# Kernel optimization log

Measured on AMD Instinct MI355X. Metric: run time of the kernel, lower is better.

## Reference

```python
import jax, jax.numpy as jnp
import numpy as np

C_IN = 1024
C_INTER = 512  # in_channels // 2, canonical NONLocalBlock default
N_CLASSES = 13


def setup_inputs() -> dict:
    key = jax.random.key(0)
    ks = jax.random.split(key, 11)
    B, T, H, W = 16, 8, 14, 14
    s = 0.02
    return {
        "x": jax.random.normal(ks[0], (B, C_IN, T, H, W), dtype=jnp.float32),
        # 1x1x1 conv projections stored as [out, in] matrices + biases
        "g_w": jax.random.normal(ks[1], (C_INTER, C_IN), dtype=jnp.float32) * s,
        "g_b": jnp.zeros((C_INTER,), dtype=jnp.float32),
        "theta_w": jax.random.normal(ks[2], (C_INTER, C_IN), dtype=jnp.float32) * s,
        "theta_b": jnp.zeros((C_INTER,), dtype=jnp.float32),
        "phi_w": jax.random.normal(ks[3], (C_INTER, C_IN), dtype=jnp.float32) * s,
        "phi_b": jnp.zeros((C_INTER,), dtype=jnp.float32),
        "w_w": jax.random.normal(ks[4], (C_IN, C_INTER), dtype=jnp.float32) * s,
        "w_b": jnp.zeros((C_IN,), dtype=jnp.float32),
        "fc_w": jax.random.normal(ks[5], (N_CLASSES, C_IN), dtype=jnp.float32) * s,
        "fc_b": jnp.zeros((N_CLASSES,), dtype=jnp.float32),
    }


def reference(x, g_w, g_b, theta_w, theta_b, phi_w, phi_b, w_w, w_b, fc_w, fc_b):
    B, C, T, H, W = x.shape
    xf = x.reshape(B, C, -1)  # [B, C, N], N = T*H*W
    # 1x1x1 conv projections == channel matmuls
    g = jnp.einsum('oc,bcn->bno', g_w, xf) + g_b        # [B, N, 512]
    th = jnp.einsum('oc,bcn->bno', theta_w, xf) + theta_b  # [B, N, 512]
    ph = jnp.einsum('oc,bcn->bno', phi_w, xf) + phi_b      # [B, N, 512]
    # pairwise affinity (embedded Gaussian): [B, N, N]
    f = jnp.einsum('bnd,bmd->bnm', th, ph)
    attn = jax.nn.softmax(f, axis=-1)
    y = jnp.einsum('bnm,bmd->bnd', attn, g)             # [B, N, 512]
    wy = jnp.einsum('cd,bnd->bcn', w_w, y) + w_b[None, :, None]  # [B, C, N]
    z = wy.reshape(B, C, T, H, W) + x                    # residual
    pooled = z.mean(axis=(2, 3, 4))                      # adaptive avgpool (1,1,1)
    return pooled @ fc_w.T + fc_b                        # [B, 13]
```

## Files before the change

kernel.cpp:

```cpp
#include <hip/hip_runtime.h>
#include <hip/hip_bf16.h>


#define BATCH 16
#define CIN   1024
#define CINT  512
#define NSP   1568
#define NPAD  1664
#define NTIL  13
#define NCLS  13

using bf16 = __hip_bfloat16;
typedef __attribute__((ext_vector_type(8))) short short8;
typedef __attribute__((ext_vector_type(4))) float f32x4;

#define DEVI static __device__ __forceinline__

DEVI void gload16(const void* g, void* l) {
  __builtin_amdgcn_global_load_lds((const __attribute__((address_space(1))) void*)g,
                                   (__attribute__((address_space(3))) void*)l, 16, 0, 0);
}

DEVI float wave_sum(float v) {
#pragma unroll
  for (int m = 32; m; m >>= 1) v += __shfl_xor(v, m);
  return v;
}

DEVI short f2bf(float f) {
  union { __hip_bfloat16 h; short s; } u;
  u.h = __float2bfloat16(f);
  return u.s;
}

__global__ __launch_bounds__(256) void k_transpose(const float* __restrict__ x,
                                                   bf16* __restrict__ xt,
                                                   float* __restrict__ xbar) {
  __shared__ float t[128 * 37];
  const int b = blockIdx.z;
  const int n0 = blockIdx.x * 32;
  const int c0 = blockIdx.y * 128;
  const int tid = threadIdx.x;
  const int lane = tid & 63;
  const float* xb = x + (size_t)b * CIN * NSP;
  const bool pad = (n0 >= NSP);
#pragma unroll
  for (int it = 0; it < 4; ++it) {
    const int slot = it * 256 + tid;
    const int cr = slot >> 3;
    const int q = slot & 7;
    float4 v = {0.f, 0.f, 0.f, 0.f};
    if (!pad) v = *(const float4*)(xb + (size_t)(c0 + cr) * NSP + n0 + q * 4);
    t[cr * 37 + q * 4 + 0] = v.x;
    t[cr * 37 + q * 4 + 1] = v.y;
    t[cr * 37 + q * 4 + 2] = v.z;
    t[cr * 37 + q * 4 + 3] = v.w;
    float s = v.x + v.y + v.z + v.w;
    s += __shfl_xor(s, 1);
    s += __shfl_xor(s, 2);
    s += __shfl_xor(s, 4);
    if ((lane & 7) == 0 && !pad)
      atomicAdd(&xbar[b * CIN + c0 + cr], s * (1.0f / NSP));
  }
  __syncthreads();
  bf16* xo = xt + (size_t)b * NPAD * CIN;
#pragma unroll
  for (int it = 0; it < 2; ++it) {
    const int slot = it * 256 + tid;
    const int n = slot >> 4;
    const int seg = slot & 15;
    short8 o;
#pragma unroll
    for (int k = 0; k < 8; ++k) o[k] = f2bf(t[(seg * 8 + k) * 37 + n]);
    *(short8*)(xo + (size_t)(n0 + n) * CIN + c0 + seg * 8) = o;
  }
}

__global__ void k_wconv(const float* __restrict__ thw, const float* __restrict__ phw,
                        bf16* __restrict__ wb) {
  const int i4 = (blockIdx.x * 256 + threadIdx.x) * 4;
  const float* s = (i4 < 512 * 1024) ? (thw + i4) : (phw + (i4 - 512 * 1024));
  const float4 v = *(const float4*)s;
  wb[i4 + 0] = __float2bfloat16(v.x);
  wb[i4 + 1] = __float2bfloat16(v.y);
  wb[i4 + 2] = __float2bfloat16(v.z);
  wb[i4 + 3] = __float2bfloat16(v.w);
}

template <int LDK>
DEVI void gemm128_bt(const bf16* Ag, const bf16* Bg, bf16* lA, bf16* lB,
                     f32x4 acc[4][4]) {
  const int tid = threadIdx.x;
  const int lane = tid & 63;
  const int w = tid >> 6;
  const int wr = (w >> 1) * 64;
  const int wc = (w & 1) * 64;
#pragma unroll 1
  for (int ks = 0; ks < LDK / 32; ++ks) {
#pragma unroll
    for (int it = 0; it < 2; ++it) {
      const int ch = w * 64 + it * 256 + lane;
      const int row = ch >> 2;
      const int kc = ch & 3;
      const int lbase = (w * 64 + it * 256) * 8;
      gload16(Ag + (size_t)row * LDK + ks * 32 + kc * 8, lA + lbase);
      gload16(Bg + (size_t)row * LDK + ks * 32 + kc * 8, lB + lbase);
    }
    __syncthreads();
    short8 af[4], bfr[4];
#pragma unroll
    for (int i = 0; i < 4; ++i)
      af[i] = *(const short8*)(lA + (wr + i * 16 + (lane & 15)) * 32 + (lane >> 4) * 8);
#pragma unroll
    for (int i = 0; i < 4; ++i)
      bfr[i] = *(const short8*)(lB + (wc + i * 16 + (lane & 15)) * 32 + (lane >> 4) * 8);
#pragma unroll
    for (int m = 0; m < 4; ++m)
#pragma unroll
      for (int n = 0; n < 4; ++n)
        acc[m][n] = __builtin_amdgcn_mfma_f32_16x16x32_bf16(af[m], bfr[n], acc[m][n], 0, 0, 0);
    __syncthreads();
  }
}

__global__ __launch_bounds__(256) void k_proj(const bf16* __restrict__ xt,
                                              const bf16* __restrict__ wb,
                                              const float* __restrict__ thb,
                                              const float* __restrict__ phb,
                                              bf16* __restrict__ th,
                                              bf16* __restrict__ ph) {
  __shared__ bf16 smem[16384];
  const int bo = blockIdx.x;
  const int bm = blockIdx.y;
  f32x4 acc[4][4];
  const f32x4 z = {0.f, 0.f, 0.f, 0.f};
#pragma unroll
  for (int m = 0; m < 4; ++m)
#pragma unroll
    for (int n = 0; n < 4; ++n) acc[m][n] = z;

  gemm128_bt<CIN>(xt + (size_t)bm * 128 * CIN, wb + (size_t)bo * 128 * CIN,
                  smem, smem + 4096, acc);

  const int tid = threadIdx.x;
  const int lane = tid & 63;
  const int w = tid >> 6;
  const int wr = (w >> 1) * 64;
  const int wc = (w & 1) * 64;
  const float* bias = (bo < 4) ? thb : phb;
  bf16* outb = (bo < 4) ? th : ph;
  const int obase = (bo & 3) * 128;
  __syncthreads();
#pragma unroll
  for (int m = 0; m < 4; ++m)
#pragma unroll
    for (int n = 0; n < 4; ++n) {
      const int col_l = wc + n * 16 + (lane & 15);
      const float bv = bias[obase + col_l];
#pragma unroll
      for (int j = 0; j < 4; ++j) {
        const int row_l = wr + m * 16 + (lane >> 4) * 4 + j;
        smem[row_l * 128 + (col_l ^ ((row_l & 7) << 3))] =
            __float2bfloat16(acc[m][n][j] + bv);
      }
    }
  __syncthreads();
#pragma unroll
  for (int it = 0; it < 8; ++it) {
    const int slot = it * 256 + tid;
    const int r = slot >> 4;
    const int seg = slot & 15;
    const short8 v = *(const short8*)(smem + r * 128 + ((seg ^ (r & 7)) << 3));
    *(short8*)(outb + (size_t)(bm * 128 + r) * CINT + obase + seg * 8) = v;
  }
}

__global__ __launch_bounds__(256) void k_fgemm(const bf16* __restrict__ th,
                                               const bf16* __restrict__ ph,
                                               bf16* __restrict__ eb,
                                               float* __restrict__ psum) {
  __shared__ bf16 smem[16384];
  __shared__ float rsum2[2][128];
  const int bn = blockIdx.x, bm = blockIdx.y, b = blockIdx.z;
  f32x4 acc[4][4];
  const f32x4 z = {0.f, 0.f, 0.f, 0.f};
#pragma unroll
  for (int m = 0; m < 4; ++m)
#pragma unroll
    for (int n = 0; n < 4; ++n) acc[m][n] = z;

  gemm128_bt<CINT>(th + ((size_t)b * NPAD + bm * 128) * CINT,
                   ph + ((size_t)b * NPAD + bn * 128) * CINT,
                   smem, smem + 4096, acc);

  const int tid = threadIdx.x;
  const int lane = tid & 63;
  const int w = tid >> 6;
  const int wr = (w >> 1) * 64;
  const int wc = (w & 1) * 64;
  __syncthreads();
#pragma unroll
  for (int m = 0; m < 4; ++m)
#pragma unroll
    for (int j = 0; j < 4; ++j) {
      const int row_l = wr + m * 16 + (lane >> 4) * 4 + j;
      float ps = 0.f;
#pragma unroll
      for (int n = 0; n < 4; ++n) {
        const int col_l = wc + n * 16 + (lane & 15);
        const float ev = __expf(acc[m][n][j]);
        smem[row_l * 128 + (col_l ^ ((row_l & 7) << 3))] = __float2bfloat16(ev);
        if (bn * 128 + col_l < NSP) ps += ev;
      }
      ps += __shfl_xor(ps, 1);
      ps += __shfl_xor(ps, 2);
      ps += __shfl_xor(ps, 4);
      ps += __shfl_xor(ps, 8);
      if ((lane & 15) == 0) rsum2[w & 1][row_l] = ps;
    }
  __syncthreads();
  if (tid < 128)
    psum[((size_t)b * NTIL + bn) * NPAD + bm * 128 + tid] =
        rsum2[0][tid] + rsum2[1][tid];
  bf16* ebb = eb + ((size_t)b * NPAD + bm * 128) * NPAD + bn * 128;
#pragma unroll
  for (int it = 0; it < 8; ++it) {
    const int slot = it * 256 + tid;
    const int r = slot >> 4;
    const int seg = slot & 15;
    const short8 v = *(const short8*)(smem + r * 128 + ((seg ^ (r & 7)) << 3));
    *(short8*)(ebb + (size_t)r * NPAD + seg * 8) = v;
  }
}

__global__ void k_recip(const float* __restrict__ psum, float* __restrict__ rinv) {
  const int id = blockIdx.x * 256 + threadIdx.x;
  const int b = id / NSP;
  const int n = id - b * NSP;
  float s = 0.f;
#pragma unroll
  for (int t = 0; t < NTIL; ++t) s += psum[((size_t)b * NTIL + t) * NPAD + n];
  rinv[id] = 1.0f / s;
}

__global__ void k_abar(const bf16* __restrict__ eb, const float* __restrict__ rinv,
                       float* __restrict__ abar) {
  const int m = blockIdx.x * 256 + threadIdx.x;
  const int b = blockIdx.z;
  const bool act = m < NSP;
  const bf16* fb = eb + (size_t)b * NPAD * NPAD;
  const int n0 = blockIdx.y * 196;
  float local = 0.f;
  for (int n = n0; n < n0 + 196; ++n) {
    const float iS = rinv[b * NSP + n];
    if (act) local += __bfloat162float(fb[(size_t)n * NPAD + m]) * iS;
  }
  if (act) atomicAdd(&abar[b * NSP + m], local * (1.0f / NSP));
}

__global__ void k_xg(const bf16* __restrict__ xt, const float* __restrict__ abar,
                     float* __restrict__ xg) {
  const int c = blockIdx.x * 256 + threadIdx.x;
  const int b = blockIdx.z;
  const bf16* xb = xt + (size_t)b * NPAD * CIN;
  const int n0 = blockIdx.y * 196;
  float s = 0.f;
  for (int n = n0; n < n0 + 196; ++n)
    s += __bfloat162float(xb[(size_t)n * CIN + c]) * abar[b * NSP + n];
  atomicAdd(&xg[b * CIN + c], s);
}

__global__ __launch_bounds__(64) void k_ybar(const float* __restrict__ gw,
                                             const float* __restrict__ gb,
                                             const float* __restrict__ xg,
                                             float* __restrict__ syb) {
  const int d = blockIdx.x;
  const int lane = threadIdx.x;
  const float4* wr = (const float4*)(gw + (size_t)d * CIN);
  float4 wv[4];
#pragma unroll
  for (int k = 0; k < 4; ++k) wv[k] = wr[k * 64 + lane];
  const float bv = gb[d];
#pragma unroll 1
  for (int b = 0; b < BATCH; ++b) {
    const float4* xr = (const float4*)(xg + (size_t)b * CIN);
    float s = 0.f;
#pragma unroll
    for (int k = 0; k < 4; ++k) {
      const float4 xv = xr[k * 64 + lane];
      s += wv[k].x * xv.x + wv[k].y * xv.y + wv[k].z * xv.z + wv[k].w * xv.w;
    }
    s = wave_sum(s);
    if (lane == 0) syb[b * CINT + d] = s + bv;
  }
}

__global__ __launch_bounds__(64) void k_spool(const float* __restrict__ ww,
                                              const float* __restrict__ wbias,
                                              const float* __restrict__ xbar,
                                              const float* __restrict__ syb,
                                              float* __restrict__ spool) {
  const int c = blockIdx.x;
  const int lane = threadIdx.x;
  const float4* wr = (const float4*)(ww + (size_t)c * CINT);
  float4 wv[2];
#pragma unroll
  for (int k = 0; k < 2; ++k) wv[k] = wr[k * 64 + lane];
  const float bv = wbias[c];
#pragma unroll 1
  for (int b = 0; b < BATCH; ++b) {
    const float4* yr = (const float4*)(syb + (size_t)b * CINT);
    float s = 0.f;
#pragma unroll
    for (int k = 0; k < 2; ++k) {
      const float4 yv = yr[k * 64 + lane];
      s += wv[k].x * yv.x + wv[k].y * yv.y + wv[k].z * yv.z + wv[k].w * yv.w;
    }
    s = wave_sum(s);
    if (lane == 0) spool[b * CIN + c] = s + bv + xbar[b * CIN + c];
  }
}

__global__ __launch_bounds__(64) void k_out(const float* __restrict__ spool,
                                            const float* __restrict__ fcw,
                                            const float* __restrict__ fcb,
                                            float* __restrict__ out) {
  const int b = blockIdx.x;
  const int lane = threadIdx.x;
  const float4* pr = (const float4*)(spool + (size_t)b * CIN);
  float4 pv[4];
#pragma unroll
  for (int k = 0; k < 4; ++k) pv[k] = pr[k * 64 + lane];
#pragma unroll 1
  for (int cls = 0; cls < NCLS; ++cls) {
    const float4* wr = (const float4*)(fcw + (size_t)cls * CIN);
    float s = 0.f;
#pragma unroll
    for (int k = 0; k < 4; ++k) {
      const float4 wv = wr[k * 64 + lane];
      s += wv.x * pv[k].x + wv.y * pv[k].y + wv.z * pv[k].z + wv.w * pv[k].w;
    }
    s = wave_sum(s);
    if (lane == 0) out[b * NCLS + cls] = s + fcb[cls];
  }
}

extern "C" void kernel_launch(void* const* d_in, const int* in_sizes, int n_in,
                              void* d_out, int out_size, void* d_ws, size_t ws_size,
                              hipStream_t stream) {
  const float* x    = (const float*)d_in[0];
  const float* g_w  = (const float*)d_in[1];
  const float* g_b  = (const float*)d_in[2];
  const float* th_w = (const float*)d_in[3];
  const float* th_b = (const float*)d_in[4];
  const float* ph_w = (const float*)d_in[5];
  const float* ph_b = (const float*)d_in[6];
  const float* w_w  = (const float*)d_in[7];
  const float* w_b  = (const float*)d_in[8];
  const float* fc_w = (const float*)d_in[9];
  const float* fc_b = (const float*)d_in[10];
  float* out = (float*)d_out;

  char* ws = (char*)d_ws;
  size_t off = 0;
  auto carve = [&](size_t bytes) {
    void* p = ws + off;
    off = (off + bytes + 255) & ~(size_t)255;
    return p;
  };
  bf16*  xt    = (bf16*)carve((size_t)BATCH * NPAD * CIN * 2);
  bf16*  wb    = (bf16*)carve((size_t)1024 * 1024 * 2);
  bf16*  th    = (bf16*)carve((size_t)BATCH * NPAD * CINT * 2);
  bf16*  ph    = (bf16*)carve((size_t)BATCH * NPAD * CINT * 2);
  bf16*  eb    = (bf16*)carve((size_t)BATCH * NPAD * NPAD * 2);
  float* psum  = (float*)carve((size_t)BATCH * NTIL * NPAD * 4);
  float* rinv  = (float*)carve((size_t)BATCH * NSP * 4);
  float* abar  = (float*)carve((size_t)BATCH * NSP * 4);
  float* xbar  = (float*)carve((size_t)BATCH * CIN * 4);
  float* xg    = (float*)carve((size_t)BATCH * CIN * 4);
  float* syb   = (float*)carve((size_t)BATCH * CINT * 4);
  float* spool = (float*)carve((size_t)BATCH * CIN * 4);
  (void)ws_size; (void)in_sizes; (void)n_in; (void)out_size;

  hipMemsetAsync(abar, 0, (size_t)BATCH * NSP * 4, stream);
  hipMemsetAsync(xbar, 0, (size_t)BATCH * CIN * 4, stream);
  hipMemsetAsync(xg,   0, (size_t)BATCH * CIN * 4, stream);

  k_transpose<<<dim3(52, 8, 16), 256, 0, stream>>>(x, xt, xbar);
  k_wconv<<<1024, 256, 0, stream>>>(th_w, ph_w, wb);
  k_proj<<<dim3(8, 208), 256, 0, stream>>>(xt, wb, th_b, ph_b, th, ph);
  k_fgemm<<<dim3(13, 13, 16), 256, 0, stream>>>(th, ph, eb, psum);
  k_recip<<<98, 256, 0, stream>>>(psum, rinv);
  k_abar<<<dim3(7, 8, 16), 256, 0, stream>>>(eb, rinv, abar);
  k_xg<<<dim3(4, 8, 16), 256, 0, stream>>>(xt, abar, xg);
  k_ybar<<<512, 64, 0, stream>>>(g_w, g_b, xg, syb);
  k_spool<<<1024, 64, 0, stream>>>(w_w, w_b, xbar, syb, spool);
  k_out<<<16, 64, 0, stream>>>(spool, fc_w, fc_b, out);
}
```

Before: 355.7 us.

## Halve LDS in proj and fgemm epilogues; remap blocks for XCD-local reuse

The k_proj and k_fgemm epilogues now stage the output tile through shared memory in two 64-row halves, so the shared buffer drops from 32KB to 16KB. The aim is to allow more resident blocks per CU. Both kernels also switch to a 1D grid whose block ids are remapped so that blocks landing on the same XCD (id mod 8) share input tiles (same bm, or same batch), to improve L2 reuse. The cost is extra barriers and a serialized two-phase epilogue.

```diff
diff --git a/kernel.cpp b/kernel.cpp
--- a/kernel.cpp
+++ b/kernel.cpp
@@ -129,9 +129,13 @@
                                               const float* __restrict__ phb,
                                               bf16* __restrict__ th,
                                               bf16* __restrict__ ph) {
-  __shared__ bf16 smem[16384];
-  const int bo = blockIdx.x;
-  const int bm = blockIdx.y;
+  __shared__ bf16 smem[8192];
+  const int id = blockIdx.x;
+  const int rcls = id & 7;
+  const int q = id >> 3;
+  const int bm = (q >> 3) * 8 + rcls;
+  const int bo = q & 7;
+
   f32x4 acc[4][4];
   const f32x4 z = {0.f, 0.f, 0.f, 0.f};
 #pragma unroll
@@ -145,33 +149,38 @@
   const int tid = threadIdx.x;
   const int lane = tid & 63;
   const int w = tid >> 6;
-  const int wr = (w >> 1) * 64;
   const int wc = (w & 1) * 64;
+  const int hsel = w >> 1;
   const float* bias = (bo < 4) ? thb : phb;
   bf16* outb = (bo < 4) ? th : ph;
   const int obase = (bo & 3) * 128;
-  __syncthreads();
-#pragma unroll
-  for (int m = 0; m < 4; ++m)
-#pragma unroll
-    for (int n = 0; n < 4; ++n) {
-      const int col_l = wc + n * 16 + (lane & 15);
-      const float bv = bias[obase + col_l];
-#pragma unroll
-      for (int j = 0; j < 4; ++j) {
-        const int row_l = wr + m * 16 + (lane >> 4) * 4 + j;
-        smem[row_l * 128 + (col_l ^ ((row_l & 7) << 3))] =
-            __float2bfloat16(acc[m][n][j] + bv);
-      }
-    }
-  __syncthreads();
-#pragma unroll
-  for (int it = 0; it < 8; ++it) {
-    const int slot = it * 256 + tid;
-    const int r = slot >> 4;
-    const int seg = slot & 15;
-    const short8 v = *(const short8*)(smem + r * 128 + ((seg ^ (r & 7)) << 3));
-    *(short8*)(outb + (size_t)(bm * 128 + r) * CINT + obase + seg * 8) = v;
+#pragma unroll
+  for (int h = 0; h < 2; ++h) {
+    __syncthreads();
+    if (hsel == h) {
+#pragma unroll
+      for (int m = 0; m < 4; ++m)
+#pragma unroll
+        for (int n = 0; n < 4; ++n) {
+          const int col_l = wc + n * 16 + (lane & 15);
+          const float bv = bias[obase + col_l];
+#pragma unroll
+          for (int j = 0; j < 4; ++j) {
+            const int lr = m * 16 + (lane >> 4) * 4 + j;
+            smem[lr * 128 + (col_l ^ ((lr & 7) << 3))] =
+                __float2bfloat16(acc[m][n][j] + bv);
+          }
+        }
+    }
+    __syncthreads();
+#pragma unroll
+    for (int it = 0; it < 4; ++it) {
+      const int slot = it * 256 + tid;
+      const int rr = slot >> 4;
+      const int seg = slot & 15;
+      const short8 v = *(const short8*)(smem + rr * 128 + ((seg ^ (rr & 7)) << 3));
+      *(short8*)(outb + (size_t)(bm * 128 + h * 64 + rr) * CINT + obase + seg * 8) = v;
+    }
   }
 }
 
@@ -179,9 +188,17 @@
                                                const bf16* __restrict__ ph,
                                                bf16* __restrict__ eb,
                                                float* __restrict__ psum) {
-  __shared__ bf16 smem[16384];
+  __shared__ bf16 smem[8192];
   __shared__ float rsum2[2][128];
-  const int bn = blockIdx.x, bm = blockIdx.y, b = blockIdx.z;
+  const int id = blockIdx.x;
+  const int rcls = id & 7;
+  const int q = id >> 3;
+  const int bloc = q / 169;
+  const int t = q - bloc * 169;
+  const int b = bloc * 8 + rcls;
+  const int bm = t / 13;
+  const int bn = t - bm * 13;
+
   f32x4 acc[4][4];
   const f32x4 z = {0.f, 0.f, 0.f, 0.f};
 #pragma unroll
@@ -196,41 +213,46 @@
   const int tid = threadIdx.x;
   const int lane = tid & 63;
   const int w = tid >> 6;
-  const int wr = (w >> 1) * 64;
   const int wc = (w & 1) * 64;
-  __syncthreads();
-#pragma unroll
-  for (int m = 0; m < 4; ++m)
-#pragma unroll
-    for (int j = 0; j < 4; ++j) {
-      const int row_l = wr + m * 16 + (lane >> 4) * 4 + j;
-      float ps = 0.f;
-#pragma unroll
-      for (int n = 0; n < 4; ++n) {
-        const int col_l = wc + n * 16 + (lane & 15);
-        const float ev = __expf(acc[m][n][j]);
-        smem[row_l * 128 + (col_l ^ ((row_l & 7) << 3))] = __float2bfloat16(ev);
-        if (bn * 128 + col_l < NSP) ps += ev;
-      }
-      ps += __shfl_xor(ps, 1);
-      ps += __shfl_xor(ps, 2);
-      ps += __shfl_xor(ps, 4);
-      ps += __shfl_xor(ps, 8);
-      if ((lane & 15) == 0) rsum2[w & 1][row_l] = ps;
-    }
-  __syncthreads();
+  const int hsel = w >> 1;
+  bf16* ebb = eb + ((size_t)b * NPAD + bm * 128) * NPAD + bn * 128;
+#pragma unroll
+  for (int h = 0; h < 2; ++h) {
+    __syncthreads();
+    if (hsel == h) {
+#pragma unroll
+      for (int m = 0; m < 4; ++m)
+#pragma unroll
+        for (int j = 0; j < 4; ++j) {
+          const int lr = m * 16 + (lane >> 4) * 4 + j;
+          float ps = 0.f;
+#pragma unroll
+          for (int n = 0; n < 4; ++n) {
+            const int col_l = wc + n * 16 + (lane & 15);
+            const float ev = __expf(acc[m][n][j]);
+            smem[lr * 128 + (col_l ^ ((lr & 7) << 3))] = __float2bfloat16(ev);
+            if (bn * 128 + col_l < NSP) ps += ev;
+          }
+          ps += __shfl_xor(ps, 1);
+          ps += __shfl_xor(ps, 2);
+          ps += __shfl_xor(ps, 4);
+          ps += __shfl_xor(ps, 8);
+          if ((lane & 15) == 0) rsum2[w & 1][h * 64 + lr] = ps;
+        }
+    }
+    __syncthreads();
+#pragma unroll
+    for (int it = 0; it < 4; ++it) {
+      const int slot = it * 256 + tid;
+      const int rr = slot >> 4;
+      const int seg = slot & 15;
+      const short8 v = *(const short8*)(smem + rr * 128 + ((seg ^ (rr & 7)) << 3));
+      *(short8*)(ebb + (size_t)(h * 64 + rr) * NPAD + seg * 8) = v;
+    }
+  }
   if (tid < 128)
     psum[((size_t)b * NTIL + bn) * NPAD + bm * 128 + tid] =
         rsum2[0][tid] + rsum2[1][tid];
-  bf16* ebb = eb + ((size_t)b * NPAD + bm * 128) * NPAD + bn * 128;
-#pragma unroll
-  for (int it = 0; it < 8; ++it) {
-    const int slot = it * 256 + tid;
-    const int r = slot >> 4;
-    const int seg = slot & 15;
-    const short8 v = *(const short8*)(smem + r * 128 + ((seg ^ (r & 7)) << 3));
-    *(short8*)(ebb + (size_t)r * NPAD + seg * 8) = v;
-  }
 }
 
 __global__ void k_recip(const float* __restrict__ psum, float* __restrict__ rinv) {
@@ -388,8 +410,8 @@
 
   k_transpose<<<dim3(52, 8, 16), 256, 0, stream>>>(x, xt, xbar);
   k_wconv<<<1024, 256, 0, stream>>>(th_w, ph_w, wb);
-  k_proj<<<dim3(8, 208), 256, 0, stream>>>(xt, wb, th_b, ph_b, th, ph);
-  k_fgemm<<<dim3(13, 13, 16), 256, 0, stream>>>(th, ph, eb, psum);
+  k_proj<<<1664, 256, 0, stream>>>(xt, wb, th_b, ph_b, th, ph);
+  k_fgemm<<<2704, 256, 0, stream>>>(th, ph, eb, psum);
   k_recip<<<98, 256, 0, stream>>>(psum, rinv);
   k_abar<<<dim3(7, 8, 16), 256, 0, stream>>>(eb, rinv, abar);
   k_xg<<<dim3(4, 8, 16), 256, 0, stream>>>(xt, abar, xg);
```

New measurement: 344.9 us. -3.1%, faster.
